# Kernel optimization log

Measured on AMD Instinct MI355X. Metric: run time of the kernel, lower is better.

Reference implementation:

```python
import jax, jax.numpy as jnp
import numpy as np

N = 50000      # nodes
E = 800000     # edges (avg degree 16)
D_IN = 16      # raw node feature dim
D = 64         # d_model
H = 8          # heads
DH = D // H    # dim_head = 8
L = 2          # num_encoder_layers
EPS = 1e-5
SCALE = float(np.sqrt(DH))


def _xavier(key, shape):
    fan_in, fan_out = shape[-2], shape[-1]
    a = float(np.sqrt(6.0 / (fan_in + fan_out)))
    return jax.random.uniform(key, shape, jnp.float32, -a, a)


def setup_inputs() -> dict:
    key = jax.random.key(0)
    ks = jax.random.split(key, 20)
    feat = jax.random.normal(ks[0], (N, D_IN), jnp.float32)
    src = jax.random.randint(ks[1], (E,), 0, N, jnp.int32)
    dst = jax.random.randint(ks[2], (E,), 0, N, jnp.int32)
    return {
        "feat": feat,
        "src": src,
        "dst": dst,
        "W_emb": _xavier(ks[3], (D_IN, D)),
        "b_emb": jnp.zeros((D,), jnp.float32),
        "Wq": _xavier(ks[4], (L, D, D)),
        "Wk": _xavier(ks[5], (L, D, D)),
        "Wv": _xavier(ks[6], (L, D, D)),
        "Wo": _xavier(ks[7], (L, D, D)),
        "bo": jnp.zeros((L, D), jnp.float32),
        "bn1_g": jnp.ones((L, D), jnp.float32),
        "bn1_b": jnp.zeros((L, D), jnp.float32),
        "W1": _xavier(ks[8], (L, D, 2 * D)),
        "b1": jnp.zeros((L, 2 * D), jnp.float32),
        "W2": _xavier(ks[9], (L, 2 * D, D)),
        "b2": jnp.zeros((L, D), jnp.float32),
        "bn2_g": jnp.ones((L, D), jnp.float32),
        "bn2_b": jnp.zeros((L, D), jnp.float32),
    }


def _batch_norm(x, g, b):
    # BatchNorm1d (training-mode forward: batch statistics, biased var)
    mu = jnp.mean(x, axis=0)
    var = jnp.var(x, axis=0)
    return (x - mu) / jnp.sqrt(var + EPS) * g + b


def _layer(h, src, dst, Wq, Wk, Wv, Wo, bo, bn1_g, bn1_b, W1, b1, W2, b2, bn2_g, bn2_b):
    h_in1 = h
    Q = (h @ Wq).reshape(N, H, DH)
    K = (h @ Wk).reshape(N, H, DH)
    V = (h @ Wv).reshape(N, H, DH)
    # SDDMM: per-edge dot(K[src], Q[dst]) -> [E, H]
    e = jnp.sum(K[src] * Q[dst], axis=-1)
    # scaled_exp: exp(clamp(score/sqrt(dh), -10, 10)) stored as edge 'score'
    e = jnp.exp(jnp.clip(e / SCALE, -10.0, 10.0))
    # reduce_func then applies a softmax over mailbox scores (double exp, faithful)
    m = jax.ops.segment_max(e, dst, num_segments=N)          # [N, H]
    w = jnp.exp(e - m[dst])                                   # [E, H]
    s = jax.ops.segment_sum(w, dst, num_segments=N)           # [N, H]
    alpha = w / s[dst]                                        # [E, H]
    out = jax.ops.segment_sum(alpha[:, :, None] * V[src], dst, num_segments=N)
    h = out.reshape(N, D) @ Wo + bo
    h = _batch_norm(h_in1 + h, bn1_g, bn1_b)
    h_in2 = h
    h = jax.nn.relu(h @ W1 + b1) @ W2 + b2
    h = _batch_norm(h + h_in2, bn2_g, bn2_b)
    return h


def reference(feat, src, dst, W_emb, b_emb, Wq, Wk, Wv, Wo, bo, bn1_g, bn1_b,
              W1, b1, W2, b2, bn2_g, bn2_b):
    h = feat @ W_emb + b_emb  # embedding_h (dropout=0)
    for l in range(L):
        h = _layer(h, src, dst, Wq[l], Wk[l], Wv[l], Wo[l], bo[l],
                   bn1_g[l], bn1_b[l], W1[l], b1[l], W2[l], b2[l],
                   bn2_g[l], bn2_b[l])
    return h
```

## Files before the change

kernel.cpp:

```cpp
#include <hip/hip_runtime.h>

#define NNODES 50000
#define NEDGES 800000
#define DM 64
#define NH 8
#define DH 8
#define EPSN 1e-5f
#define INV_SCALE 0.3535533905932738f
#define SCAN_BLOCKS 200
#define SCAN_CHUNK  250
#define DCAP 128

template<int KA, int KB, int R, bool RELU, bool RES, bool STATS>
__global__ __launch_bounds__(256, 2) void gemm_k(const float* __restrict__ A,
    const float* __restrict__ W, int woff,
    const float* __restrict__ bias, int boff,
    float* __restrict__ C, float* __restrict__ stats, int Nrows)
{
    constexpr int CG   = KB / 4;
    constexpr int RG   = 256 / CG;
    constexpr int ROWS = RG * R;
    constexpr int APAD = KA + 4;
    constexpr int KAq  = KA / 4;

    __shared__ __align__(16) float sW[KA * KB];
    __shared__ __align__(16) float sA[ROWS * APAD];

    const int tid  = threadIdx.x;
    const int row0 = blockIdx.x * ROWS;

    for (int i4 = tid; i4 < KA * KB / 4; i4 += 256)
        *(float4*)&sW[i4 * 4] = ((const float4*)(W + woff))[i4];
    for (int i4 = tid; i4 < ROWS * KAq; i4 += 256) {
        int r = i4 / KAq, kq = i4 - r * KAq;
        int gr = row0 + r;
        float4 v = make_float4(0.f, 0.f, 0.f, 0.f);
        if (gr < Nrows) v = ((const float4*)A)[(size_t)gr * KAq + kq];
        *(float4*)&sA[r * APAD + kq * 4] = v;
    }
    __syncthreads();

    const int cg = tid % CG, rg = tid / CG;
    const int c0 = cg * 4, r0 = rg * R;

    float4 acc[R];
#pragma unroll
    for (int rr = 0; rr < R; rr++) acc[rr] = make_float4(0.f, 0.f, 0.f, 0.f);

#pragma unroll 2
    for (int k = 0; k < KA; k += 4) {
        float4 w0 = *(const float4*)&sW[(k + 0) * KB + c0];
        float4 w1 = *(const float4*)&sW[(k + 1) * KB + c0];
        float4 w2 = *(const float4*)&sW[(k + 2) * KB + c0];
        float4 w3 = *(const float4*)&sW[(k + 3) * KB + c0];
#pragma unroll
        for (int rr = 0; rr < R; rr++) {
            float4 av = *(const float4*)&sA[(r0 + rr) * APAD + k];
            acc[rr].x += av.x * w0.x + av.y * w1.x + av.z * w2.x + av.w * w3.x;
            acc[rr].y += av.x * w0.y + av.y * w1.y + av.z * w2.y + av.w * w3.y;
            acc[rr].z += av.x * w0.z + av.y * w1.z + av.z * w2.z + av.w * w3.z;
            acc[rr].w += av.x * w0.w + av.y * w1.w + av.z * w2.w + av.w * w3.w;
        }
    }

    float4 bv = make_float4(0.f, 0.f, 0.f, 0.f);
    if (bias) {
        bv.x = bias[boff + c0];     bv.y = bias[boff + c0 + 1];
        bv.z = bias[boff + c0 + 2]; bv.w = bias[boff + c0 + 3];
    }

    float4 vals[R];
#pragma unroll
    for (int rr = 0; rr < R; rr++) {
        int grow = row0 + r0 + rr;
        bool valid = grow < Nrows;
        float4 v;
        v.x = acc[rr].x + bv.x; v.y = acc[rr].y + bv.y;
        v.z = acc[rr].z + bv.z; v.w = acc[rr].w + bv.w;
        if (RELU) {
            v.x = fmaxf(v.x, 0.f); v.y = fmaxf(v.y, 0.f);
            v.z = fmaxf(v.z, 0.f); v.w = fmaxf(v.w, 0.f);
        }
        if (valid) {
            if (RES) {
                float4 old = *(const float4*)&C[(size_t)grow * KB + c0];
                v.x += old.x; v.y += old.y; v.z += old.z; v.w += old.w;
            }
            *(float4*)&C[(size_t)grow * KB + c0] = v;
        } else {
            v = make_float4(0.f, 0.f, 0.f, 0.f);
        }
        vals[rr] = v;
    }

    if (STATS) {
        __syncthreads();
        float4 cs = make_float4(0.f, 0.f, 0.f, 0.f);
#pragma unroll
        for (int rr = 0; rr < R; rr++) {
            cs.x += vals[rr].x; cs.y += vals[rr].y;
            cs.z += vals[rr].z; cs.w += vals[rr].w;
        }
        *(float4*)&sA[rg * KB + c0] = cs;
        __syncthreads();
        if (tid < KB) {
            float s = 0.f;
#pragma unroll
            for (int g = 0; g < RG; g++) s += sA[g * KB + tid];
            atomicAdd(&stats[tid], s);
        }
        __syncthreads();
        float4 cq = make_float4(0.f, 0.f, 0.f, 0.f);
#pragma unroll
        for (int rr = 0; rr < R; rr++) {
            cq.x += vals[rr].x * vals[rr].x; cq.y += vals[rr].y * vals[rr].y;
            cq.z += vals[rr].z * vals[rr].z; cq.w += vals[rr].w * vals[rr].w;
        }
        *(float4*)&sA[rg * KB + c0] = cq;
        __syncthreads();
        if (tid < KB) {
            float s = 0.f;
#pragma unroll
            for (int g = 0; g < RG; g++) s += sA[g * KB + tid];
            atomicAdd(&stats[KB + tid], s);
        }
    }
}

__global__ __launch_bounds__(256, 2) void qkv_k(const float* __restrict__ A,
    const float* __restrict__ Wq, const float* __restrict__ Wk,
    const float* __restrict__ Wv, int woff,
    float* __restrict__ Qo, float* __restrict__ Ko, float* __restrict__ Vo,
    int Nrows)
{
    constexpr int APAD = 68;
    __shared__ __align__(16) float sW[64 * 64];
    __shared__ __align__(16) float sA[64 * APAD];

    const int tid  = threadIdx.x;
    const int row0 = blockIdx.x * 64;

    for (int i4 = tid; i4 < 64 * 16; i4 += 256) {
        int r = i4 >> 4, kq = i4 & 15;
        int gr = row0 + r;
        float4 v = make_float4(0.f, 0.f, 0.f, 0.f);
        if (gr < Nrows) v = ((const float4*)A)[(size_t)gr * 16 + kq];
        *(float4*)&sA[r * APAD + kq * 4] = v;
    }

    const float* Ws[3]   = {Wq, Wk, Wv};
    float*       Outs[3] = {Qo, Ko, Vo};

    const int cg = tid & 15, rg = tid >> 4;
    const int c0 = cg * 4, r0 = rg * 4;

    for (int m = 0; m < 3; m++) {
        __syncthreads();
        for (int i4 = tid; i4 < 1024; i4 += 256)
            *(float4*)&sW[i4 * 4] = ((const float4*)(Ws[m] + woff))[i4];
        __syncthreads();

        float4 acc[4];
#pragma unroll
        for (int rr = 0; rr < 4; rr++) acc[rr] = make_float4(0.f, 0.f, 0.f, 0.f);

#pragma unroll 2
        for (int k = 0; k < 64; k += 4) {
            float4 w0 = *(const float4*)&sW[(k + 0) * 64 + c0];
            float4 w1 = *(const float4*)&sW[(k + 1) * 64 + c0];
            float4 w2 = *(const float4*)&sW[(k + 2) * 64 + c0];
            float4 w3 = *(const float4*)&sW[(k + 3) * 64 + c0];
#pragma unroll
            for (int rr = 0; rr < 4; rr++) {
                float4 av = *(const float4*)&sA[(r0 + rr) * APAD + k];
                acc[rr].x += av.x * w0.x + av.y * w1.x + av.z * w2.x + av.w * w3.x;
                acc[rr].y += av.x * w0.y + av.y * w1.y + av.z * w2.y + av.w * w3.y;
                acc[rr].z += av.x * w0.z + av.y * w1.z + av.z * w2.z + av.w * w3.z;
                acc[rr].w += av.x * w0.w + av.y * w1.w + av.z * w2.w + av.w * w3.w;
            }
        }

#pragma unroll
        for (int rr = 0; rr < 4; rr++) {
            int grow = row0 + r0 + rr;
            if (grow < Nrows)
                *(float4*)&Outs[m][(size_t)grow * 64 + c0] = acc[rr];
        }
    }
}

__global__ __launch_bounds__(256) void bn_apply(const float* __restrict__ Hin,
    float* __restrict__ Hout, const float* __restrict__ stats,
    const float* __restrict__ g, int goff, const float* __restrict__ b, int boff)
{
    int i = blockIdx.x * 256 + threadIdx.x;
    if (i >= NNODES * DM) return;
    int c = i & 63;
    float mu  = stats[c] * (1.0f / NNODES);
    float var = stats[64 + c] * (1.0f / NNODES) - mu * mu;
    float istd = rsqrtf(fmaxf(var, 0.0f) + EPSN);
    Hout[i] = (Hin[i] - mu) * istd * g[goff + c] + b[boff + c];
}

__global__ __launch_bounds__(256) void zero_int_k(int* __restrict__ p, int n)
{
    int i = blockIdx.x * 256 + threadIdx.x;
    if (i < n) p[i] = 0;
}

__global__ __launch_bounds__(256) void count_k(const int* __restrict__ dst,
                                               int* __restrict__ cursor)
{
    int e = blockIdx.x * 256 + threadIdx.x;
    if (e < NEDGES) atomicAdd(&cursor[dst[e]], 1);
}

__global__ __launch_bounds__(256) void csr_scanA(const int* __restrict__ cursor,
                                                 int* __restrict__ bsum)
{
    __shared__ int red[256];
    const int base = blockIdx.x * SCAN_CHUNK;
    int s = 0;
    for (int i = threadIdx.x; i < SCAN_CHUNK; i += 256) s += cursor[base + i];
    red[threadIdx.x] = s;
    __syncthreads();
    for (int o = 128; o > 0; o >>= 1) {
        if (threadIdx.x < o) red[threadIdx.x] += red[threadIdx.x + o];
        __syncthreads();
    }
    if (threadIdx.x == 0) bsum[blockIdx.x] = red[0];
}

__global__ __launch_bounds__(256) void csr_scanB(int* __restrict__ bsum)
{
    __shared__ int t[256];
    const int tid = threadIdx.x;
    int v = (tid < SCAN_BLOCKS) ? bsum[tid] : 0;
    t[tid] = v;
    __syncthreads();
    for (int off = 1; off < 256; off <<= 1) {
        int x = (tid >= off) ? t[tid - off] : 0;
        __syncthreads();
        t[tid] += x;
        __syncthreads();
    }
    if (tid < SCAN_BLOCKS) bsum[tid] = t[tid] - v;
}

__global__ __launch_bounds__(256) void csr_scanC(int* __restrict__ cursor,
    int* __restrict__ rowptr, const int* __restrict__ bsum)
{
    __shared__ int t[256];
    const int base = blockIdx.x * SCAN_CHUNK;
    const int tid  = threadIdx.x;
    int deg = (tid < SCAN_CHUNK) ? cursor[base + tid] : 0;
    t[tid] = deg;
    __syncthreads();
    for (int off = 1; off < 256; off <<= 1) {
        int x = (tid >= off) ? t[tid - off] : 0;
        __syncthreads();
        t[tid] += x;
        __syncthreads();
    }
    int excl = bsum[blockIdx.x] + t[tid] - deg;
    if (tid < SCAN_CHUNK) {
        rowptr[base + tid] = excl;
        cursor[base + tid] = excl;
    }
    if (blockIdx.x == 0 && tid == 0) rowptr[NNODES] = NEDGES;
}

__global__ __launch_bounds__(256) void fill_k(const int* __restrict__ src,
    const int* __restrict__ dst, int* __restrict__ cursor,
    int* __restrict__ nbr)
{
    int e = blockIdx.x * 256 + threadIdx.x;
    if (e >= NEDGES) return;
    int pos = atomicAdd(&cursor[dst[e]], 1);
    nbr[pos] = src[e];
}

__global__ __launch_bounds__(256) void attn_fused_k(const float* __restrict__ Q,
    const float* __restrict__ K, const float* __restrict__ V,
    const int* __restrict__ rowptr, const int* __restrict__ nbr,
    float* __restrict__ U)
{
    __shared__ float sS[4][DCAP * NH];
    __shared__ int   sN[4][DCAP];

    const int w = threadIdx.x >> 6;
    const int d = blockIdx.x * 4 + w;
    if (d >= NNODES) return;
    const int t = threadIdx.x & 63;
    const int h = t >> 3;
    const int e0 = rowptr[d], e1 = rowptr[d + 1];
    const int deg = e1 - e0;
    const float q = Q[(size_t)d * DM + t];
    float* myS = sS[w];
    int*   myN = sN[w];

    if (deg <= DCAP) {
        float m = 0.0f;
        int p = e0;
        for (; p + 2 <= e1; p += 2) {
            int s0 = nbr[p], s1 = nbr[p + 1];
            float kv0 = K[(size_t)s0 * DM + t] * q;
            float kv1 = K[(size_t)s1 * DM + t] * q;
            kv0 += __shfl_xor(kv0, 1, 64);  kv1 += __shfl_xor(kv1, 1, 64);
            kv0 += __shfl_xor(kv0, 2, 64);  kv1 += __shfl_xor(kv1, 2, 64);
            kv0 += __shfl_xor(kv0, 4, 64);  kv1 += __shfl_xor(kv1, 4, 64);
            float ev0 = __expf(fminf(fmaxf(kv0 * INV_SCALE, -10.f), 10.f));
            float ev1 = __expf(fminf(fmaxf(kv1 * INV_SCALE, -10.f), 10.f));
            m = fmaxf(m, fmaxf(ev0, ev1));
            if ((t & 7) == 0) {
                myS[(p - e0) * NH + h]     = ev0;
                myS[(p + 1 - e0) * NH + h] = ev1;
            }
            if (t == 0) { myN[p - e0] = s0; myN[p + 1 - e0] = s1; }
        }
        if (p < e1) {
            int s0 = nbr[p];
            float kv0 = K[(size_t)s0 * DM + t] * q;
            kv0 += __shfl_xor(kv0, 1, 64);
            kv0 += __shfl_xor(kv0, 2, 64);
            kv0 += __shfl_xor(kv0, 4, 64);
            float ev0 = __expf(fminf(fmaxf(kv0 * INV_SCALE, -10.f), 10.f));
            m = fmaxf(m, ev0);
            if ((t & 7) == 0) myS[(p - e0) * NH + h] = ev0;
            if (t == 0)       myN[p - e0] = s0;
        }

        float S = 0.0f, u = 0.0f;
        int i = 0;
        for (; i + 2 <= deg; i += 2) {
            int s0 = myN[i], s1 = myN[i + 1];
            float v0 = V[(size_t)s0 * DM + t];
            float v1 = V[(size_t)s1 * DM + t];
            float w0 = __expf(myS[i * NH + h] - m);
            float w1 = __expf(myS[(i + 1) * NH + h] - m);
            S += w0 + w1;
            u += w0 * v0 + w1 * v1;
        }
        if (i < deg) {
            int s0 = myN[i];
            float w0 = __expf(myS[i * NH + h] - m);
            S += w0;
            u += w0 * V[(size_t)s0 * DM + t];
        }
        U[(size_t)d * DM + t] = (S > 0.f) ? u / S : 0.f;
    } else {
        float m = 0.0f, S = 0.0f, u = 0.0f;
        for (int p = e0; p < e1; p++) {
            int s = nbr[p];
            float kv = K[(size_t)s * DM + t] * q;
            float v  = V[(size_t)s * DM + t];
            kv += __shfl_xor(kv, 1, 64);
            kv += __shfl_xor(kv, 2, 64);
            kv += __shfl_xor(kv, 4, 64);
            float ev = __expf(fminf(fmaxf(kv * INV_SCALE, -10.f), 10.f));
            float mn = fmaxf(m, ev);
            float r  = __expf(m - mn);
            float w0 = __expf(ev - mn);
            S = S * r + w0;
            u = u * r + w0 * v;
            m = mn;
        }
        U[(size_t)d * DM + t] = (S > 0.f) ? u / S : 0.f;
    }
}

__global__ __launch_bounds__(256) void fill_const_k(float* __restrict__ out, int n)
{
    int i = blockIdx.x * 256 + threadIdx.x;
    if (i < n) out[i] = 100.0f;
}

extern "C" void kernel_launch(void* const* d_in, const int* in_sizes, int n_in,
                              void* d_out, int out_size, void* d_ws, size_t ws_size,
                              hipStream_t stream)
{
    const int expect[18] = {800000, 800000, 800000, 1024, 64,
                            8192, 8192, 8192, 8192, 128,
                            128, 128, 16384, 256, 16384, 128, 128, 128};
    bool order_ok = (n_in == 18) && (out_size == NNODES * DM);
    if (order_ok)
        for (int i = 0; i < 18; i++)
            if (in_sizes[i] != expect[i]) { order_ok = false; break; }
    if (!order_ok) {
        fill_const_k<<<(out_size + 255) / 256, 256, 0, stream>>>((float*)d_out,
                                                                 out_size);
        return;
    }

    const float* feat  = (const float*)d_in[0];
    const int*   src   = (const int*)d_in[1];
    const int*   dst   = (const int*)d_in[2];
    const float* W_emb = (const float*)d_in[3];
    const float* b_emb = (const float*)d_in[4];
    const float* Wq    = (const float*)d_in[5];
    const float* Wk    = (const float*)d_in[6];
    const float* Wv    = (const float*)d_in[7];
    const float* Wo    = (const float*)d_in[8];
    const float* bo    = (const float*)d_in[9];
    const float* bn1_g = (const float*)d_in[10];
    const float* bn1_b = (const float*)d_in[11];
    const float* W1    = (const float*)d_in[12];
    const float* b1    = (const float*)d_in[13];
    const float* W2    = (const float*)d_in[14];
    const float* b2    = (const float*)d_in[15];
    const float* bn2_g = (const float*)d_in[16];
    const float* bn2_b = (const float*)d_in[17];

    const size_t ND = (size_t)NNODES * DM;
    float* ws     = (float*)d_ws;
    float* Hb     = ws;
    float* Qb     = Hb + ND;
    float* Kb     = Qb + ND;
    float* Vb     = Kb + ND;
    float* Ub     = Vb + ND;
    float* stats  = Ub + ND;
    int*   rowptr = (int*)(stats + 256);
    int*   cursor = rowptr + (NNODES + 1);
    int*   bsum   = cursor + NNODES;
    int*   nbr    = bsum + SCAN_BLOCKS;
    float* Fb     = Qb;

    const size_t BASE = (5 * ND + 256) * 4
                      + ((NNODES + 1) + NNODES + SCAN_BLOCKS + NEDGES) * 4;
    if (ws_size < BASE) {
        fill_const_k<<<(out_size + 255) / 256, 256, 0, stream>>>((float*)d_out,
                                                                 out_size);
        return;
    }

    const int g64 = (NNODES + 63) / 64;
    const int g32 = (NNODES + 31) / 32;
    const int gND = (int)(ND / 256);
    const int gE  = (NEDGES + 255) / 256;
    const int gAT = (NNODES + 3) / 4;

    zero_int_k<<<(NNODES + 255) / 256, 256, 0, stream>>>(cursor, NNODES);
    count_k<<<gE, 256, 0, stream>>>(dst, cursor);
    csr_scanA<<<SCAN_BLOCKS, 256, 0, stream>>>(cursor, bsum);
    csr_scanB<<<1, 256, 0, stream>>>(bsum);
    csr_scanC<<<SCAN_BLOCKS, 256, 0, stream>>>(cursor, rowptr, bsum);
    fill_k<<<gE, 256, 0, stream>>>(src, dst, cursor, nbr);

    gemm_k<16, 64, 4, false, false, false>
        <<<g64, 256, 0, stream>>>(feat, W_emb, 0, b_emb, 0, Hb, nullptr, NNODES);

    for (int l = 0; l < 2; l++) {
        const int woff  = l * DM * DM;
        const int w1off = l * DM * 2 * DM;
        const int boff  = l * DM;
        const int b1off = l * 2 * DM;

        qkv_k<<<g64, 256, 0, stream>>>(Hb, Wq, Wk, Wv, woff, Qb, Kb, Vb, NNODES);

        attn_fused_k<<<gAT, 256, 0, stream>>>(Qb, Kb, Vb, rowptr, nbr, Ub);

        hipMemsetAsync(stats, 0, 128 * 4, stream);
        gemm_k<64, 64, 4, false, true, true>
            <<<g64, 256, 0, stream>>>(Ub, Wo, woff, bo, boff, Hb, stats, NNODES);
        bn_apply<<<gND, 256, 0, stream>>>(Hb, Hb, stats, bn1_g, boff, bn1_b, boff);

        gemm_k<64, 128, 4, true, false, false>
            <<<g32, 256, 0, stream>>>(Hb, W1, w1off, b1, b1off, Fb, nullptr, NNODES);
        hipMemsetAsync(stats, 0, 128 * 4, stream);
        gemm_k<128, 64, 2, false, true, true>
            <<<g32, 256, 0, stream>>>(Fb, W2, w1off, b2, boff, Hb, stats, NNODES);
        float* outp = (l == 1) ? (float*)d_out : Hb;
        bn_apply<<<gND, 256, 0, stream>>>(Hb, outp, stats, bn2_g, boff, bn2_b, boff);
    }
}
```

Baseline: 673.4 us.

## Process 16 edges per wavefront iteration with per-head lanes and online softmax

Restructures the per-node attention kernel so each lane owns one head and one edge slot, processing 16 edges per iteration with float4 loads of K and V rows. The dot product is computed in-register instead of through shuffles. A single-pass online softmax replaces the two-pass shared-memory scheme, and a cross-lane butterfly reduction combines the partial sums at the end. This removes shared-memory staging and the serialized per-edge loop. In exchange each lane holds 8 accumulators, the end needs many shuffles, and lanes sit idle when degree is not a multiple of 16.

```diff
diff --git a/kernel.cpp b/kernel.cpp
--- a/kernel.cpp
+++ b/kernel.cpp
@@ -9,7 +9,6 @@
 #define INV_SCALE 0.3535533905932738f
 #define SCAN_BLOCKS 200
 #define SCAN_CHUNK  250
-#define DCAP 128
 
 template<int KA, int KB, int R, bool RELU, bool RES, bool STATS>
 __global__ __launch_bounds__(256, 2) void gemm_k(const float* __restrict__ A,
@@ -285,88 +284,83 @@
     const int* __restrict__ rowptr, const int* __restrict__ nbr,
     float* __restrict__ U)
 {
-    __shared__ float sS[4][DCAP * NH];
-    __shared__ int   sN[4][DCAP];
-
     const int w = threadIdx.x >> 6;
     const int d = blockIdx.x * 4 + w;
     if (d >= NNODES) return;
-    const int t = threadIdx.x & 63;
-    const int h = t >> 3;
+    const int l  = threadIdx.x & 63;
+    const int el = l >> 3;
+    const int h  = l & 7;
     const int e0 = rowptr[d], e1 = rowptr[d + 1];
     const int deg = e1 - e0;
-    const float q = Q[(size_t)d * DM + t];
-    float* myS = sS[w];
-    int*   myN = sN[w];
-
-    if (deg <= DCAP) {
-        float m = 0.0f;
-        int p = e0;
-        for (; p + 2 <= e1; p += 2) {
-            int s0 = nbr[p], s1 = nbr[p + 1];
-            float kv0 = K[(size_t)s0 * DM + t] * q;
-            float kv1 = K[(size_t)s1 * DM + t] * q;
-            kv0 += __shfl_xor(kv0, 1, 64);  kv1 += __shfl_xor(kv1, 1, 64);
-            kv0 += __shfl_xor(kv0, 2, 64);  kv1 += __shfl_xor(kv1, 2, 64);
-            kv0 += __shfl_xor(kv0, 4, 64);  kv1 += __shfl_xor(kv1, 4, 64);
-            float ev0 = __expf(fminf(fmaxf(kv0 * INV_SCALE, -10.f), 10.f));
-            float ev1 = __expf(fminf(fmaxf(kv1 * INV_SCALE, -10.f), 10.f));
-            m = fmaxf(m, fmaxf(ev0, ev1));
-            if ((t & 7) == 0) {
-                myS[(p - e0) * NH + h]     = ev0;
-                myS[(p + 1 - e0) * NH + h] = ev1;
-            }
-            if (t == 0) { myN[p - e0] = s0; myN[p + 1 - e0] = s1; }
-        }
-        if (p < e1) {
-            int s0 = nbr[p];
-            float kv0 = K[(size_t)s0 * DM + t] * q;
-            kv0 += __shfl_xor(kv0, 1, 64);
-            kv0 += __shfl_xor(kv0, 2, 64);
-            kv0 += __shfl_xor(kv0, 4, 64);
-            float ev0 = __expf(fminf(fmaxf(kv0 * INV_SCALE, -10.f), 10.f));
-            m = fmaxf(m, ev0);
-            if ((t & 7) == 0) myS[(p - e0) * NH + h] = ev0;
-            if (t == 0)       myN[p - e0] = s0;
-        }
-
-        float S = 0.0f, u = 0.0f;
-        int i = 0;
-        for (; i + 2 <= deg; i += 2) {
-            int s0 = myN[i], s1 = myN[i + 1];
-            float v0 = V[(size_t)s0 * DM + t];
-            float v1 = V[(size_t)s1 * DM + t];
-            float w0 = __expf(myS[i * NH + h] - m);
-            float w1 = __expf(myS[(i + 1) * NH + h] - m);
-            S += w0 + w1;
-            u += w0 * v0 + w1 * v1;
-        }
-        if (i < deg) {
-            int s0 = myN[i];
-            float w0 = __expf(myS[i * NH + h] - m);
-            S += w0;
-            u += w0 * V[(size_t)s0 * DM + t];
-        }
-        U[(size_t)d * DM + t] = (S > 0.f) ? u / S : 0.f;
-    } else {
-        float m = 0.0f, S = 0.0f, u = 0.0f;
-        for (int p = e0; p < e1; p++) {
-            int s = nbr[p];
-            float kv = K[(size_t)s * DM + t] * q;
-            float v  = V[(size_t)s * DM + t];
-            kv += __shfl_xor(kv, 1, 64);
-            kv += __shfl_xor(kv, 2, 64);
-            kv += __shfl_xor(kv, 4, 64);
-            float ev = __expf(fminf(fmaxf(kv * INV_SCALE, -10.f), 10.f));
-            float mn = fmaxf(m, ev);
-            float r  = __expf(m - mn);
-            float w0 = __expf(ev - mn);
-            S = S * r + w0;
-            u = u * r + w0 * v;
-            m = mn;
-        }
-        U[(size_t)d * DM + t] = (S > 0.f) ? u / S : 0.f;
-    }
+
+    if (deg == 0) {
+        U[(size_t)d * DM + h * DH + el] = 0.f;
+        return;
+    }
+
+    const float4* qp = (const float4*)(Q + (size_t)d * DM + h * DH);
+    const float4 q0 = qp[0], q1 = qp[1];
+
+    float m = 0.0f;
+    float S = 0.0f;
+    float u[8] = {0.f, 0.f, 0.f, 0.f, 0.f, 0.f, 0.f, 0.f};
+
+    for (int base = 0; base < deg; base += 16) {
+        const int i0 = base + el, i1 = base + 8 + el;
+        const bool v0ok = i0 < deg, v1ok = i1 < deg;
+        const int s0 = nbr[e0 + (v0ok ? i0 : 0)];
+        const int s1 = nbr[e0 + (v1ok ? i1 : 0)];
+
+        const float4* kp0 = (const float4*)(K + (size_t)s0 * DM + h * DH);
+        const float4* vp0 = (const float4*)(V + (size_t)s0 * DM + h * DH);
+        const float4* kp1 = (const float4*)(K + (size_t)s1 * DM + h * DH);
+        const float4* vp1 = (const float4*)(V + (size_t)s1 * DM + h * DH);
+        float4 ka0 = kp0[0], ka1 = kp0[1];
+        float4 kb0 = kp1[0], kb1 = kp1[1];
+        float4 va0 = vp0[0], va1 = vp0[1];
+        float4 vb0 = vp1[0], vb1 = vp1[1];
+
+        float d0 = ka0.x * q0.x + ka0.y * q0.y + ka0.z * q0.z + ka0.w * q0.w
+                 + ka1.x * q1.x + ka1.y * q1.y + ka1.z * q1.z + ka1.w * q1.w;
+        float d1 = kb0.x * q0.x + kb0.y * q0.y + kb0.z * q0.z + kb0.w * q0.w
+                 + kb1.x * q1.x + kb1.y * q1.y + kb1.z * q1.z + kb1.w * q1.w;
+
+        float ev0 = __expf(fminf(fmaxf(d0 * INV_SCALE, -10.f), 10.f));
+        float ev1 = __expf(fminf(fmaxf(d1 * INV_SCALE, -10.f), 10.f));
+        if (!v0ok) ev0 = 0.f;
+        if (!v1ok) ev1 = 0.f;
+
+        float bm = fmaxf(ev0, ev1);
+        bm = fmaxf(bm, __shfl_xor(bm, 8, 64));
+        bm = fmaxf(bm, __shfl_xor(bm, 16, 64));
+        bm = fmaxf(bm, __shfl_xor(bm, 32, 64));
+
+        const float mn = fmaxf(m, bm);
+        const float r  = __expf(m - mn);
+        const float w0 = v0ok ? __expf(ev0 - mn) : 0.f;
+        const float w1 = v1ok ? __expf(ev1 - mn) : 0.f;
+
+        S = S * r + w0 + w1;
+        u[0] = u[0] * r + w0 * va0.x + w1 * vb0.x;
+        u[1] = u[1] * r + w0 * va0.y + w1 * vb0.y;
+        u[2] = u[2] * r + w0 * va0.z + w1 * vb0.z;
+        u[3] = u[3] * r + w0 * va0.w + w1 * vb0.w;
+        u[4] = u[4] * r + w0 * va1.x + w1 * vb1.x;
+        u[5] = u[5] * r + w0 * va1.y + w1 * vb1.y;
+        u[6] = u[6] * r + w0 * va1.z + w1 * vb1.z;
+        u[7] = u[7] * r + w0 * va1.w + w1 * vb1.w;
+        m = mn;
+    }
+
+#pragma unroll
+    for (int off = 8; off <= 32; off <<= 1) {
+        S += __shfl_xor(S, off, 64);
+#pragma unroll
+        for (int j = 0; j < 8; j++) u[j] += __shfl_xor(u[j], off, 64);
+    }
+
+    const float out = (S > 0.f) ? u[el] / S : 0.f;
+    U[(size_t)d * DM + h * DH + el] = out;
 }
 
 __global__ __launch_bounds__(256) void fill_const_k(float* __restrict__ out, int n)
```

Result: faster. 605.1 us (-10.1%).
